# Optimization experiments

Hardware: AMD Instinct MI355X
Metric: run time of the kernel (lower is better)

Reference implementation:

```python
import jax, jax.numpy as jnp
import numpy as np

EMBED_DIM = 1024
NUM_HEADS = 16
HEAD_DIM = EMBED_DIM // NUM_HEADS
INV_SQRT_DIM = 1.0 / np.sqrt(EMBED_DIM).astype(np.float32)  # note: embed_dim, not head_dim


def setup_inputs() -> dict:
    key = jax.random.key(0)
    k1, k2 = jax.random.split(key)
    hidden_states = jax.random.normal(k1, (2, 2048, EMBED_DIM), dtype=jnp.float32)
    # nn.Linear(embed_dim, 3*embed_dim, bias=False); store as [in, out] so y = x @ w_qkv
    w_qkv = jax.random.normal(k2, (EMBED_DIM, 3 * EMBED_DIM), dtype=jnp.float32) * 0.02
    return {"hidden_states": hidden_states, "w_qkv": w_qkv}


def reference(hidden_states, w_qkv):
    b, s, _ = hidden_states.shape
    qkv = hidden_states @ w_qkv  # [b, s, 3*E]
    q, k, v = jnp.split(qkv, 3, axis=-1)

    def split_heads(x):  # [b, s, E] -> [b, h, s, d]
        return x.reshape(b, s, NUM_HEADS, HEAD_DIM).transpose(0, 2, 1, 3)

    q, k, v = split_heads(q), split_heads(k), split_heads(v)
    scores = jnp.einsum('bhqd,bhkd->bhqk', q, k) * INV_SQRT_DIM
    w = jax.nn.softmax(scores, axis=-1)
    out = jnp.einsum('bhqk,bhkd->bhqd', w, v)  # [b, h, s, d]
    return out.transpose(0, 2, 1, 3).reshape(b, s, EMBED_DIM)
```

## Files before the change

kernel.cpp:

```cpp
#include <hip/hip_runtime.h>
#include <stdint.h>


typedef __attribute__((ext_vector_type(8))) short v8s;
typedef __attribute__((ext_vector_type(4))) float v4f;

__device__ __forceinline__ unsigned short bf16bits(float f) {
  union { float f; unsigned int u; } c; c.f = f;
  unsigned int u = c.u;
  unsigned int r = (u + 0x7fffu + ((u >> 16) & 1u)) >> 16;
  return (unsigned short)r;
}

__device__ __forceinline__ v4f mfma16(v8s a, v8s b, v4f c) {
  return __builtin_amdgcn_mfma_f32_16x16x32_bf16(a, b, c, 0, 0, 0);
}

#define GLD16(g, l) __builtin_amdgcn_global_load_lds( \
    (const __attribute__((address_space(1))) unsigned int*)(g), \
    (__attribute__((address_space(3))) unsigned int*)(l), 16, 0, 0)

__global__ __launch_bounds__(256) void cvt_x_kernel(const float4* __restrict__ x4,
                                                    ushort4* __restrict__ o4, int n4) {
  int i = blockIdx.x * 256 + threadIdx.x;
  if (i < n4) {
    float4 v = x4[i];
    ushort4 o;
    o.x = bf16bits(v.x); o.y = bf16bits(v.y); o.z = bf16bits(v.z); o.w = bf16bits(v.w);
    o4[i] = o;
  }
}

__global__ __launch_bounds__(256) void cvt_wT_kernel(const float* __restrict__ w,
                                                     unsigned short* __restrict__ wt) {
  __shared__ float t[32][33];
  int n0 = blockIdx.x * 32, k0 = blockIdx.y * 32;
  int tx = threadIdx.x & 31, ty = threadIdx.x >> 5;
  for (int i = 0; i < 4; ++i) {
    int kr = ty + i * 8;
    t[kr][tx] = w[(k0 + kr) * 3072 + n0 + tx];
  }
  __syncthreads();
  for (int i = 0; i < 4; ++i) {
    int nr = ty + i * 8;
    wt[(n0 + nr) * 1024 + k0 + tx] = bf16bits(t[tx][nr]);
  }
}

__global__ __launch_bounds__(256) void qkv_gemm(const unsigned short* __restrict__ A,
                                                const unsigned short* __restrict__ Bm,
                                                unsigned short* __restrict__ Cq,
                                                unsigned short* __restrict__ VTh) {
  __shared__ __align__(16) unsigned short S[24576];
  int bm = blockIdx.x, bn = blockIdx.y;
  int tid = threadIdx.x, lane = tid & 63, wave = tid >> 6;
  int wr = wave >> 1, wc = wave & 1;

  v4f acc[2][4];
  for (int i = 0; i < 2; ++i)
    for (int j = 0; j < 4; ++j) acc[i][j] = (v4f){0.f, 0.f, 0.f, 0.f};

  auto STAGE = [&](int h, int kk) {
    unsigned short* As = S + h * 12288;
    unsigned short* Bs = As + 4096;
    for (int i = 0; i < 2; ++i) {
      int e = i * 256 + tid;
      int row = e >> 3, cc = e & 7;
      int sc = cc ^ (row & 7);
      GLD16(A + (bm * 64 + row) * 1024 + kk + sc * 8,
            (char*)As + (i * 256 + wave * 64) * 16);
    }
    for (int i = 0; i < 4; ++i) {
      int e = i * 256 + tid;
      int row = e >> 3, cc = e & 7;
      int sc = cc ^ (row & 7);
      GLD16(Bm + (bn * 128 + row) * 1024 + kk + sc * 8,
            (char*)Bs + (i * 256 + wave * 64) * 16);
    }
  };
  auto COMPUTE = [&](int h) {
    const unsigned short* As = S + h * 12288;
    const unsigned short* Bs = As + 4096;
    for (int ks = 0; ks < 2; ++ks) {
      v8s af[2], bf[4];
      for (int rt = 0; rt < 2; ++rt) {
        int ra = wr * 32 + rt * 16 + (lane & 15);
        int ca = (ks * 4 + (lane >> 4)) ^ (ra & 7);
        af[rt] = *(const v8s*)&As[ra * 64 + ca * 8];
      }
      for (int ct = 0; ct < 4; ++ct) {
        int rb = wc * 64 + ct * 16 + (lane & 15);
        int cb = (ks * 4 + (lane >> 4)) ^ (rb & 7);
        bf[ct] = *(const v8s*)&Bs[rb * 64 + cb * 8];
      }
      for (int rt = 0; rt < 2; ++rt)
        for (int ct = 0; ct < 4; ++ct)
          acc[rt][ct] = mfma16(af[rt], bf[ct], acc[rt][ct]);
    }
  };

  STAGE(0, 0);
  __syncthreads();
  for (int kt = 0; kt < 15; ++kt) {
    STAGE((kt + 1) & 1, (kt + 1) * 64);
    COMPUTE(kt & 1);
    __syncthreads();
  }
  COMPUTE(1);
  __syncthreads();

  if (bn < 16) {
    for (int ct = 0; ct < 4; ++ct) {
      int col = wc * 64 + ct * 16 + (lane & 15);
      for (int rt = 0; rt < 2; ++rt)
        for (int j = 0; j < 4; ++j) {
          int m = wr * 32 + rt * 16 + ((lane >> 4) << 2) + j;
          S[m * 128 + (((col >> 3) ^ (m & 7)) << 3) + (col & 7)] = bf16bits(acc[rt][ct][j]);
        }
    }
    __syncthreads();
    for (int i = 0; i < 4; ++i) {
      int c = i * 256 + tid;
      int m = c >> 4, c8 = c & 15;
      v8s v = *(const v8s*)&S[m * 128 + ((c8 ^ (m & 7)) << 3)];
      *(v8s*)&Cq[(size_t)(bm * 64 + m) * 2048 + bn * 128 + c8 * 8] = v;
    }
  } else {
    for (int ct = 0; ct < 4; ++ct) {
      int n = wc * 64 + ct * 16 + (lane & 15);
      for (int rt = 0; rt < 2; ++rt) {
        int m0 = wr * 32 + rt * 16 + ((lane >> 4) << 2);
        ushort4 p4;
        p4.x = bf16bits(acc[rt][ct][0]); p4.y = bf16bits(acc[rt][ct][1]);
        p4.z = bf16bits(acc[rt][ct][2]); p4.w = bf16bits(acc[rt][ct][3]);
        *(ushort4*)&S[n * 64 + (((m0 >> 3) ^ (n & 7)) << 3) + (m0 & 7)] = p4;
      }
    }
    __syncthreads();
    int b = bm >> 5, s0 = (bm & 31) * 64;
    for (int i = 0; i < 4; ++i) {
      int c = i * 256 + tid;
      int n = c >> 3, c8 = c & 7;
      v8s v = *(const v8s*)&S[n * 64 + ((c8 ^ (n & 7)) << 3)];
      int nn = bn * 128 + n - 2048;
      int head = nn >> 6, d = nn & 63;
      *(v8s*)&VTh[(size_t)((b * 16 + head) * 64 + d) * 2048 + s0 + c8 * 8] = v;
    }
  }
}

__global__ __launch_bounds__(256) void attn_kernel(const unsigned short* __restrict__ Cq,
                                                   const unsigned short* __restrict__ VTh,
                                                   float* __restrict__ out) {
  __shared__ __align__(16) unsigned short Qs[64 * 64];
  __shared__ __align__(16) unsigned short Ks[2][64 * 64];
  __shared__ __align__(16) unsigned short Vs[2][64 * 64];
  __shared__ __align__(16) unsigned short Ps[64 * 64];
  int qb = blockIdx.x, bh = blockIdx.y;
  int tid = threadIdx.x, lane = tid & 63, wave = tid >> 6;
  int wq = wave * 16;
  int b = bh >> 4, h = bh & 15;

  const unsigned short* Qg = Cq + (size_t)(b * 2048 + qb * 64) * 2048 + h * 64;
  const unsigned short* Kg = Cq + (size_t)(b * 2048) * 2048 + 1024 + h * 64;
  const unsigned short* Vg = VTh + (size_t)bh * 64 * 2048;

  for (int i = 0; i < 2; ++i) {
    int e = i * 256 + tid;
    int row = e >> 3, cc = e & 7;
    int sc = cc ^ (row & 7);
    GLD16(Qg + (size_t)row * 2048 + sc * 8, (char*)Qs + (i * 256 + wave * 64) * 16);
    GLD16(Kg + (size_t)row * 2048 + sc * 8, (char*)Ks[0] + (i * 256 + wave * 64) * 16);
    GLD16(Vg + row * 2048 + sc * 8, (char*)Vs[0] + (i * 256 + wave * 64) * 16);
  }
  __syncthreads();

  v8s qf[2];
  for (int ks = 0; ks < 2; ++ks) {
    int rq = wq + (lane & 15);
    int cq = (ks * 4 + (lane >> 4)) ^ (rq & 7);
    qf[ks] = *(const v8s*)&Qs[rq * 64 + cq * 8];
  }

  v4f oacc[4];
  for (int j = 0; j < 4; ++j) oacc[j] = (v4f){0.f, 0.f, 0.f, 0.f};
  float rsum[4] = {};

  for (int kt = 0; kt < 32; ++kt) {
    int cur = kt & 1;
    if (kt < 31) {
      for (int i = 0; i < 2; ++i) {
        int e = i * 256 + tid;
        int row = e >> 3, cc = e & 7;
        int sc = cc ^ (row & 7);
        GLD16(Kg + (size_t)((kt + 1) * 64 + row) * 2048 + sc * 8,
              (char*)Ks[cur ^ 1] + (i * 256 + wave * 64) * 16);
        GLD16(Vg + row * 2048 + (kt + 1) * 64 + sc * 8,
              (char*)Vs[cur ^ 1] + (i * 256 + wave * 64) * 16);
      }
    }

    v4f sacc[4];
    for (int j = 0; j < 4; ++j) sacc[j] = (v4f){0.f, 0.f, 0.f, 0.f};
    for (int ks = 0; ks < 2; ++ks) {
      v8s kf[4];
      for (int ct = 0; ct < 4; ++ct) {
        int rk = ct * 16 + (lane & 15);
        int ck = (ks * 4 + (lane >> 4)) ^ (rk & 7);
        kf[ct] = *(const v8s*)&Ks[cur][rk * 64 + ck * 8];
      }
      for (int ct = 0; ct < 4; ++ct)
        sacc[ct] = mfma16(qf[ks], kf[ct], sacc[ct]);
    }

    for (int ct = 0; ct < 4; ++ct)
      for (int j = 0; j < 4; ++j) {
        float p = __expf(sacc[ct][j] * 0.03125f);
        rsum[j] += p;
        union { float f; unsigned int u; } cv; cv.f = p;
        int prow = wq + ((lane >> 4) << 2) + j;
        int col = ct * 16 + (lane & 15);
        Ps[prow * 64 + (((col >> 3) ^ (prow & 7)) << 3) + (col & 7)] =
            (unsigned short)(cv.u >> 16);
      }

    for (int ks4 = 0; ks4 < 2; ++ks4) {
      v8s pa, vb[4];
      int rp = wq + (lane & 15);
      int cp = (ks4 * 4 + (lane >> 4)) ^ (rp & 7);
      pa = *(const v8s*)&Ps[rp * 64 + cp * 8];
      for (int dt = 0; dt < 4; ++dt) {
        int rv = dt * 16 + (lane & 15);
        int cv2 = (ks4 * 4 + (lane >> 4)) ^ (rv & 7);
        vb[dt] = *(const v8s*)&Vs[cur][rv * 64 + cv2 * 8];
      }
      for (int dt = 0; dt < 4; ++dt)
        oacc[dt] = mfma16(pa, vb[dt], oacc[dt]);
    }
    __syncthreads();
  }

  for (int j = 0; j < 4; ++j) {
    float v = rsum[j];
    v += __shfl_xor(v, 1, 64);
    v += __shfl_xor(v, 2, 64);
    v += __shfl_xor(v, 4, 64);
    v += __shfl_xor(v, 8, 64);
    rsum[j] = v;
  }

  for (int dt = 0; dt < 4; ++dt) {
    int q = qb * 64 + wq + ((lane >> 4) << 2);
    int d = h * 64 + dt * 16 + (lane & 15);
    for (int j = 0; j < 4; ++j)
      out[(size_t)(b * 2048 + q + j) * 1024 + d] = oacc[dt][j] / rsum[j];
  }
}

extern "C" void kernel_launch(void* const* d_in, const int* in_sizes, int n_in,
                              void* d_out, int out_size, void* d_ws, size_t ws_size,
                              hipStream_t stream) {
  const float* x = (const float*)d_in[0];
  const float* w = (const float*)d_in[1];
  float* out = (float*)d_out;

  char* ws = (char*)d_ws;
  unsigned short* xb = (unsigned short*)ws;
  unsigned short* wT = (unsigned short*)(ws + 8388608);
  unsigned short* Cq = (unsigned short*)(ws + 14680064);
  unsigned short* VT = (unsigned short*)(ws + 31457280);

  cvt_x_kernel<<<4096, 256, 0, stream>>>((const float4*)x, (ushort4*)xb, 1048576);
  cvt_wT_kernel<<<dim3(96, 32), 256, 0, stream>>>(w, wT);
  qkv_gemm<<<dim3(64, 24), 256, 0, stream>>>(xb, wT, Cq, VT);
  attn_kernel<<<dim3(32, 32), 256, 0, stream>>>(Cq, VT, out);
}
```

Before: 189.6 us.

## Rewrite attention with 32x32 MFMA, register-resident P, and prescaled Q

The attention kernel now handles 128 queries per block with 32x32x16 bf16 MFMAs. It computes S transposed so the exponentiated probabilities can be packed with cvt_pk and permlane32_swap straight into A-operand registers, which removes the LDS round trip for P. The softmax scale and log2(e) are folded into Q inside the GEMM epilogue so the kernel can use exp2 directly. The block index is swizzled for locality. K/V double buffering is dropped in favour of single buffers with two barriers per tile, which risks exposing load latency.

Result: faster. 156.2 us (-17.6%).

```diff
diff --git a/kernel.cpp b/kernel.cpp
--- a/kernel.cpp
+++ b/kernel.cpp
@@ -4,6 +4,7 @@
 
 typedef __attribute__((ext_vector_type(8))) short v8s;
 typedef __attribute__((ext_vector_type(4))) float v4f;
+typedef __attribute__((ext_vector_type(16))) float f32x16;
 
 __device__ __forceinline__ unsigned short bf16bits(float f) {
   union { float f; unsigned int u; } c; c.f = f;
@@ -14,6 +15,23 @@
 
 __device__ __forceinline__ v4f mfma16(v8s a, v8s b, v4f c) {
   return __builtin_amdgcn_mfma_f32_16x16x32_bf16(a, b, c, 0, 0, 0);
+}
+__device__ __forceinline__ f32x16 mfma32(v8s a, v8s b, f32x16 c) {
+  return __builtin_amdgcn_mfma_f32_32x32x16_bf16(a, b, c, 0, 0, 0);
+}
+__device__ __forceinline__ f32x16 zero16() {
+  f32x16 z;
+#pragma unroll
+  for (int i = 0; i < 16; ++i) z[i] = 0.f;
+  return z;
+}
+__device__ __forceinline__ unsigned int cvtpk(float lo, float hi) {
+  unsigned int r;
+  asm("v_cvt_pk_bf16_f32 %0, %1, %2" : "=v"(r) : "v"(lo), "v"(hi));
+  return r;
+}
+__device__ __forceinline__ void pl32swap(unsigned int& a, unsigned int& b) {
+  asm volatile("v_permlane32_swap_b32 %0, %1" : "+v"(a), "+v"(b));
 }
 
 #define GLD16(g, l) __builtin_amdgcn_global_load_lds( \
@@ -60,8 +78,8 @@
   for (int i = 0; i < 2; ++i)
     for (int j = 0; j < 4; ++j) acc[i][j] = (v4f){0.f, 0.f, 0.f, 0.f};
 
-  auto STAGE = [&](int h, int kk) {
-    unsigned short* As = S + h * 12288;
+  auto STAGE = [&](int hh, int kk) {
+    unsigned short* As = S + hh * 12288;
     unsigned short* Bs = As + 4096;
     for (int i = 0; i < 2; ++i) {
       int e = i * 256 + tid;
@@ -78,8 +96,8 @@
             (char*)Bs + (i * 256 + wave * 64) * 16);
     }
   };
-  auto COMPUTE = [&](int h) {
-    const unsigned short* As = S + h * 12288;
+  auto COMPUTE = [&](int hh) {
+    const unsigned short* As = S + hh * 12288;
     const unsigned short* Bs = As + 4096;
     for (int ks = 0; ks < 2; ++ks) {
       v8s af[2], bf[4];
@@ -110,12 +128,14 @@
   __syncthreads();
 
   if (bn < 16) {
+    float qs = (bn < 8) ? 0.0450842200f : 1.0f;
     for (int ct = 0; ct < 4; ++ct) {
       int col = wc * 64 + ct * 16 + (lane & 15);
       for (int rt = 0; rt < 2; ++rt)
         for (int j = 0; j < 4; ++j) {
           int m = wr * 32 + rt * 16 + ((lane >> 4) << 2) + j;
-          S[m * 128 + (((col >> 3) ^ (m & 7)) << 3) + (col & 7)] = bf16bits(acc[rt][ct][j]);
+          S[m * 128 + (((col >> 3) ^ (m & 7)) << 3) + (col & 7)] =
+              bf16bits(acc[rt][ct][j] * qs);
         }
     }
     __syncthreads();
@@ -152,108 +172,106 @@
 __global__ __launch_bounds__(256) void attn_kernel(const unsigned short* __restrict__ Cq,
                                                    const unsigned short* __restrict__ VTh,
                                                    float* __restrict__ out) {
-  __shared__ __align__(16) unsigned short Qs[64 * 64];
-  __shared__ __align__(16) unsigned short Ks[2][64 * 64];
-  __shared__ __align__(16) unsigned short Vs[2][64 * 64];
-  __shared__ __align__(16) unsigned short Ps[64 * 64];
-  int qb = blockIdx.x, bh = blockIdx.y;
+  __shared__ __align__(16) unsigned short Qs[128 * 64];
+  __shared__ __align__(16) unsigned short Ks[64 * 64];
+  __shared__ __align__(16) unsigned short Vs[64 * 64];
   int tid = threadIdx.x, lane = tid & 63, wave = tid >> 6;
-  int wq = wave * 16;
-  int b = bh >> 4, h = bh & 15;
-
-  const unsigned short* Qg = Cq + (size_t)(b * 2048 + qb * 64) * 2048 + h * 64;
-  const unsigned short* Kg = Cq + (size_t)(b * 2048) * 2048 + 1024 + h * 64;
+  int ln31 = lane & 31, h = lane >> 5;
+  int wq = wave * 32;
+  int flat = blockIdx.x + (blockIdx.y << 4);
+  int swz = (flat & 7) * 64 + (flat >> 3);
+  int qb = swz & 15, bh = swz >> 4;
+  int b = bh >> 4, hH = bh & 15;
+
+  const unsigned short* Qg = Cq + (size_t)(b * 2048 + qb * 128) * 2048 + hH * 64;
+  const unsigned short* Kg = Cq + (size_t)(b * 2048) * 2048 + 1024 + hH * 64;
   const unsigned short* Vg = VTh + (size_t)bh * 64 * 2048;
 
-  for (int i = 0; i < 2; ++i) {
+  for (int i = 0; i < 4; ++i) {
     int e = i * 256 + tid;
     int row = e >> 3, cc = e & 7;
     int sc = cc ^ (row & 7);
     GLD16(Qg + (size_t)row * 2048 + sc * 8, (char*)Qs + (i * 256 + wave * 64) * 16);
-    GLD16(Kg + (size_t)row * 2048 + sc * 8, (char*)Ks[0] + (i * 256 + wave * 64) * 16);
-    GLD16(Vg + row * 2048 + sc * 8, (char*)Vs[0] + (i * 256 + wave * 64) * 16);
-  }
-  __syncthreads();
-
-  v8s qf[2];
-  for (int ks = 0; ks < 2; ++ks) {
-    int rq = wq + (lane & 15);
-    int cq = (ks * 4 + (lane >> 4)) ^ (rq & 7);
+  }
+  __syncthreads();
+
+  v8s qf[4];
+#pragma unroll
+  for (int ks = 0; ks < 4; ++ks) {
+    int rq = wq + ln31;
+    int cq = (ks * 2 + h) ^ (rq & 7);
     qf[ks] = *(const v8s*)&Qs[rq * 64 + cq * 8];
   }
 
-  v4f oacc[4];
-  for (int j = 0; j < 4; ++j) oacc[j] = (v4f){0.f, 0.f, 0.f, 0.f};
-  float rsum[4] = {};
+  f32x16 acc0 = zero16(), acc1 = zero16();
+  float rsum = 0.f;
 
   for (int kt = 0; kt < 32; ++kt) {
-    int cur = kt & 1;
-    if (kt < 31) {
-      for (int i = 0; i < 2; ++i) {
-        int e = i * 256 + tid;
-        int row = e >> 3, cc = e & 7;
-        int sc = cc ^ (row & 7);
-        GLD16(Kg + (size_t)((kt + 1) * 64 + row) * 2048 + sc * 8,
-              (char*)Ks[cur ^ 1] + (i * 256 + wave * 64) * 16);
-        GLD16(Vg + row * 2048 + (kt + 1) * 64 + sc * 8,
-              (char*)Vs[cur ^ 1] + (i * 256 + wave * 64) * 16);
-      }
-    }
-
-    v4f sacc[4];
-    for (int j = 0; j < 4; ++j) sacc[j] = (v4f){0.f, 0.f, 0.f, 0.f};
-    for (int ks = 0; ks < 2; ++ks) {
-      v8s kf[4];
-      for (int ct = 0; ct < 4; ++ct) {
-        int rk = ct * 16 + (lane & 15);
-        int ck = (ks * 4 + (lane >> 4)) ^ (rk & 7);
-        kf[ct] = *(const v8s*)&Ks[cur][rk * 64 + ck * 8];
-      }
-      for (int ct = 0; ct < 4; ++ct)
-        sacc[ct] = mfma16(qf[ks], kf[ct], sacc[ct]);
-    }
-
-    for (int ct = 0; ct < 4; ++ct)
-      for (int j = 0; j < 4; ++j) {
-        float p = __expf(sacc[ct][j] * 0.03125f);
-        rsum[j] += p;
-        union { float f; unsigned int u; } cv; cv.f = p;
-        int prow = wq + ((lane >> 4) << 2) + j;
-        int col = ct * 16 + (lane & 15);
-        Ps[prow * 64 + (((col >> 3) ^ (prow & 7)) << 3) + (col & 7)] =
-            (unsigned short)(cv.u >> 16);
-      }
-
-    for (int ks4 = 0; ks4 < 2; ++ks4) {
-      v8s pa, vb[4];
-      int rp = wq + (lane & 15);
-      int cp = (ks4 * 4 + (lane >> 4)) ^ (rp & 7);
-      pa = *(const v8s*)&Ps[rp * 64 + cp * 8];
-      for (int dt = 0; dt < 4; ++dt) {
-        int rv = dt * 16 + (lane & 15);
-        int cv2 = (ks4 * 4 + (lane >> 4)) ^ (rv & 7);
-        vb[dt] = *(const v8s*)&Vs[cur][rv * 64 + cv2 * 8];
-      }
-      for (int dt = 0; dt < 4; ++dt)
-        oacc[dt] = mfma16(pa, vb[dt], oacc[dt]);
-    }
-    __syncthreads();
-  }
-
-  for (int j = 0; j < 4; ++j) {
-    float v = rsum[j];
-    v += __shfl_xor(v, 1, 64);
-    v += __shfl_xor(v, 2, 64);
-    v += __shfl_xor(v, 4, 64);
-    v += __shfl_xor(v, 8, 64);
-    rsum[j] = v;
-  }
-
-  for (int dt = 0; dt < 4; ++dt) {
-    int q = qb * 64 + wq + ((lane >> 4) << 2);
-    int d = h * 64 + dt * 16 + (lane & 15);
-    for (int j = 0; j < 4; ++j)
-      out[(size_t)(b * 2048 + q + j) * 1024 + d] = oacc[dt][j] / rsum[j];
+    __syncthreads();
+    for (int i = 0; i < 2; ++i) {
+      int e = i * 256 + tid;
+      int row = e >> 3, cc = e & 7;
+      int sc = cc ^ (row & 7);
+      GLD16(Kg + (size_t)(kt * 64 + row) * 2048 + sc * 8,
+            (char*)Ks + (i * 256 + wave * 64) * 16);
+    }
+    for (int i = 0; i < 2; ++i) {
+      int e = i * 256 + tid;
+      int row = e >> 3, cc = e & 7;
+      int sc = cc ^ (row & 7);
+      GLD16(Vg + row * 2048 + kt * 64 + sc * 8, (char*)Vs + (i * 256 + wave * 64) * 16);
+    }
+    __syncthreads();
+
+    f32x16 s0 = zero16(), s1 = zero16();
+#pragma unroll
+    for (int ks = 0; ks < 4; ++ks) {
+      int ck = (ks * 2 + h) ^ (ln31 & 7);
+      v8s kf0 = *(const v8s*)&Ks[ln31 * 64 + ck * 8];
+      v8s kf1 = *(const v8s*)&Ks[(32 + ln31) * 64 + ck * 8];
+      s0 = mfma32(kf0, qf[ks], s0);
+      s1 = mfma32(kf1, qf[ks], s1);
+    }
+
+#pragma unroll
+    for (int mt = 0; mt < 2; ++mt) {
+      const f32x16 st = mt ? s1 : s0;
+      float p[16];
+#pragma unroll
+      for (int r = 0; r < 16; ++r) { p[r] = __builtin_amdgcn_exp2f(st[r]); rsum += p[r]; }
+      unsigned int w0 = cvtpk(p[0], p[1]),  w1 = cvtpk(p[2], p[3]);
+      unsigned int w2 = cvtpk(p[4], p[5]),  w3 = cvtpk(p[6], p[7]);
+      unsigned int w4 = cvtpk(p[8], p[9]),  w5 = cvtpk(p[10], p[11]);
+      unsigned int w6 = cvtpk(p[12], p[13]), w7 = cvtpk(p[14], p[15]);
+      pl32swap(w0, w2); pl32swap(w1, w3);
+      pl32swap(w4, w6); pl32swap(w5, w7);
+      union { unsigned int u[4]; v8s v; } pa0, pa1;
+      pa0.u[0] = w0; pa0.u[1] = w1; pa0.u[2] = w2; pa0.u[3] = w3;
+      pa1.u[0] = w4; pa1.u[1] = w5; pa1.u[2] = w6; pa1.u[3] = w7;
+#pragma unroll
+      for (int s = 0; s < 2; ++s) {
+        v8s pa = s ? pa1.v : pa0.v;
+        int cb = mt * 4 + s * 2 + h;
+        int rv0 = ln31, rv1 = 32 + ln31;
+        v8s vb0 = *(const v8s*)&Vs[rv0 * 64 + ((cb ^ (rv0 & 7))) * 8];
+        v8s vb1 = *(const v8s*)&Vs[rv1 * 64 + ((cb ^ (rv1 & 7))) * 8];
+        acc0 = mfma32(pa, vb0, acc0);
+        acc1 = mfma32(pa, vb1, acc1);
+      }
+    }
+  }
+
+  float rtot = rsum + __shfl_xor(rsum, 32, 64);
+  float inv = 1.0f / rtot;
+
+  int qbase = qb * 128 + wq;
+#pragma unroll
+  for (int r = 0; r < 16; ++r) {
+    int qr = (r & 3) + 8 * (r >> 2) + 4 * h;
+    float ivr = __shfl(inv, qr, 64);
+    size_t o = (size_t)(b * 2048 + qbase + qr) * 1024 + hH * 64 + ln31;
+    out[o] = acc0[r] * ivr;
+    out[o + 32] = acc1[r] * ivr;
   }
 }
 
@@ -273,5 +291,5 @@
   cvt_x_kernel<<<4096, 256, 0, stream>>>((const float4*)x, (ushort4*)xb, 1048576);
   cvt_wT_kernel<<<dim3(96, 32), 256, 0, stream>>>(w, wT);
   qkv_gemm<<<dim3(64, 24), 256, 0, stream>>>(xb, wT, Cq, VT);
-  attn_kernel<<<dim3(32, 32), 256, 0, stream>>>(Cq, VT, out);
-}
+  attn_kernel<<<dim3(16, 32), 256, 0, stream>>>(Cq, VT, out);
+}
```
